# Optimization experiments

Hardware: AMD Instinct MI355X
Metric: run time of the kernel (lower is better)

## Reference

```python
import jax, jax.numpy as jnp
import numpy as np

N_HOST = 50000
N_FLOW = 200000
D = 128
D_OUT = 32
E = 1_000_000
L = 2


def setup_inputs() -> dict:
    key = jax.random.key(0)
    ks = jax.random.split(key, 12)
    s = 0.05  # keep activations well-scaled across layers
    return {
        "x_host": jax.random.normal(ks[0], (N_HOST, D), jnp.float32),
        "x_flow": jax.random.normal(ks[1], (N_FLOW, D), jnp.float32),
        "ehf_src": jax.random.randint(ks[2], (E,), 0, N_HOST),
        "ehf_dst": jax.random.randint(ks[3], (E,), 0, N_FLOW),
        "efh_src": jax.random.randint(ks[4], (E,), 0, N_FLOW),
        "efh_dst": jax.random.randint(ks[5], (E,), 0, N_HOST),
        "Wl": jax.random.normal(ks[6], (L, 2, D, D), jnp.float32) * s,
        "bl": jax.random.normal(ks[7], (L, 2, D), jnp.float32) * s,
        "Wr": jax.random.normal(ks[8], (L, 2, D, D), jnp.float32) * s,
        "br": jax.random.normal(ks[9], (L, 2, D), jnp.float32) * s,
        "W_out": jax.random.normal(ks[10], (D, D_OUT), jnp.float32) * s,
        "b_out": jax.random.normal(ks[11], (D_OUT,), jnp.float32) * s,
    }


def _sage(x_src, x_dst, src, dst, n_dst, wl, bll, wr, brr):
    # SAGEConv (bipartite, mean aggr): lin_l(mean_{j->i} x_src[j]) + lin_r(x_dst[i])
    msg = x_src[src]                                         # [E, D] gather
    agg = jax.ops.segment_sum(msg, dst, num_segments=n_dst)  # [n_dst, D] scatter-add
    cnt = jax.ops.segment_sum(jnp.ones((src.shape[0], 1), x_src.dtype), dst,
                              num_segments=n_dst)
    mean = agg / jnp.maximum(cnt, 1.0)
    return mean @ wl + bll + x_dst @ wr + brr


def reference(x_host, x_flow, ehf_src, ehf_dst, efh_src, efh_dst,
              Wl, bl, Wr, br, W_out, b_out):
    h, f = x_host, x_flow
    for l in range(L):
        # ('host','to','flow') -> updates flow; ('flow','to','host') -> updates host
        nf = _sage(h, f, ehf_src, ehf_dst, N_FLOW, Wl[l, 0], bl[l, 0], Wr[l, 0], br[l, 0])
        nh = _sage(f, h, efh_src, efh_dst, N_HOST, Wl[l, 1], bl[l, 1], Wr[l, 1], br[l, 1])
        f = jax.nn.leaky_relu(nf)  # negative_slope 0.01, matches F.leaky_relu default
        h = jax.nn.leaky_relu(nh)
    return f @ W_out + b_out
```

## Files before the change

kernel.cpp:

```cpp
#include <hip/hip_runtime.h>
#include <stdint.h>

#define N_HOST 50000
#define N_FLOW 200000
#define DIM 128
#define DOUTN 32
#define NEDGE 1000000
#define NLAYER 2

#define GSH_F 8
#define GSH_H 6
#define NB_F ((N_FLOW + (1 << GSH_F) - 1) >> GSH_F)
#define NB_H ((N_HOST + (1 << GSH_H) - 1) >> GSH_H)
#define BCAP 2048
#define AST 136

#define CAST_FBLK 25000
#define CAST_HBLK 6250
#define ZOFF  (CAST_FBLK + CAST_HBLK)
#define ZBLK  13
#define RW_OFF (ZOFF + ZBLK)
#define RO_OFF (RW_OFF + 64)
#define PREP_GRID (RO_OFF + 2)

typedef __bf16 bf16;
typedef __bf16 bf16x4 __attribute__((ext_vector_type(4)));
typedef __bf16 bf16x8 __attribute__((ext_vector_type(8)));
typedef float floatx2 __attribute__((ext_vector_type(2)));
typedef float floatx4 __attribute__((ext_vector_type(4)));
typedef int intx4 __attribute__((ext_vector_type(4)));

__global__ __launch_bounds__(256)
void prep_all_k(const float* __restrict__ xf, const float* __restrict__ xh,
                const float* __restrict__ Wl, const float* __restrict__ Wr,
                const float* __restrict__ Wo,
                bf16* __restrict__ fA, bf16* __restrict__ hAB,
                int* __restrict__ bcnt2,
                bf16* __restrict__ WlF, bf16* __restrict__ WrF,
                bf16* __restrict__ WoF) {
    int bid = blockIdx.x;
    int t = threadIdx.x;
    if (bid < CAST_FBLK) {
        int i = (bid * 256 + t) * 4;
        float4 v = *(const float4*)(xf + i);
        bf16x4 o;
        o[0] = (bf16)v.x; o[1] = (bf16)v.y; o[2] = (bf16)v.z; o[3] = (bf16)v.w;
        *(bf16x4*)(fA + i) = o;
    } else if (bid < ZOFF) {
        int i = ((bid - CAST_FBLK) * 256 + t) * 4;
        float4 v = *(const float4*)(xh + i);
        bf16x4 o;
        o[0] = (bf16)v.x; o[1] = (bf16)v.y; o[2] = (bf16)v.z; o[3] = (bf16)v.w;
        int row = i >> 7, col = i & 127;
        *(bf16x4*)(hAB + row * 256 + col) = o;
    } else if (bid < RW_OFF) {
        int base = (bid - ZOFF) * 2048;
#pragma unroll
        for (int j = 0; j < 8; ++j) {
            int i = base + j * 256 + t;
            if (i < (NB_F + NB_H) * 16) bcnt2[i] = 0;
        }
    } else if (bid < RO_OFF) {
        int b = bid - RW_OFF;
        int y = b >> 3;
        int x = b & 7;
        int lane = t & 63;
        int w = x * 4 + (t >> 6);
        int ct = w >> 2, k0q = w & 3;
        int quad = lane >> 4, m = lane & 15;
        int mat = y & 3;
        const float* W = (y < 4 ? Wl : Wr) + (size_t)mat * DIM * DIM;
        bf16* out = (y < 4 ? WlF : WrF) + (size_t)mat * DIM * DIM;
        bf16x8 o;
#pragma unroll
        for (int j = 0; j < 8; ++j) o[j] = (bf16)W[(k0q * 32 + quad * 8 + j) * DIM + ct * 16 + m];
        *(bf16x8*)(out + ((ct * 4 + k0q) * 64 + lane) * 8) = o;
    } else {
        int b2 = bid - RO_OFF;
        int lane = t & 63;
        int w = b2 * 4 + (t >> 6);
        int ct = w >> 2, k0q = w & 3;
        int quad = lane >> 4, m = lane & 15;
        bf16x8 o;
#pragma unroll
        for (int j = 0; j < 8; ++j) o[j] = (bf16)Wo[(k0q * 32 + quad * 8 + j) * DOUTN + ct * 16 + m];
        *(bf16x8*)(WoF + ((ct * 4 + k0q) * 64 + lane) * 8) = o;
    }
}

__global__ __launch_bounds__(256)
void bucket_scatter2_k(const int* __restrict__ sF, const int* __restrict__ dF,
                       const int* __restrict__ sH, const int* __restrict__ dH,
                       int* bcntF, int* bcntH,
                       int* __restrict__ bkF, int* __restrict__ bkH) {
    int dir = blockIdx.y;
    const int* src = dir ? sH : sF;
    const int* dst = dir ? dH : dF;
    int* bcnt = dir ? bcntH : bcntF;
    int* bkey = dir ? bkH : bkF;
    int gsh = dir ? GSH_H : GSH_F;
    int e = blockIdx.x * 256 + threadIdx.x;
    if (e < NEDGE) {
        int d = dst[e];
        int b = d >> gsh;
        int p = atomicAdd(&bcnt[b << 4], 1);
        if (p < BCAP) bkey[(b << 11) + p] = (src[e] << 8) | (d & ((1 << gsh) - 1));
    }
}

__global__ __launch_bounds__(256)
void bucket_sort2_k(const int* __restrict__ bcntF, const int* __restrict__ bcntH,
                    const int* __restrict__ bkF, const int* __restrict__ bkH,
                    int2* __restrict__ rsF2, int2* __restrict__ rsH2,
                    int* __restrict__ esF, int* __restrict__ esH) {
    __shared__ int cnts[256];
    __shared__ int sd[256];
    __shared__ int ldsout[BCAP];
    int dir = blockIdx.y;
    const int* bcnt = dir ? bcntH : bcntF;
    const int* bkey = dir ? bkH : bkF;
    int2* rs2 = dir ? rsH2 : rsF2;
    int* es = dir ? esH : esF;
    int gsh = dir ? GSH_H : GSH_F;
    int b = blockIdx.x, t = threadIdx.x;
    int G = 1 << gsh;
    int base = b << 11;
    int cnt = bcnt[b << 4];
    if (cnt > BCAP) cnt = BCAP;
    int keys[8]; int nk = 0;
    for (int i = t; i < cnt; i += 256) keys[nk++] = bkey[base + i];
    cnts[t] = 0;
    __syncthreads();
    for (int j = 0; j < nk; ++j) atomicAdd(&cnts[keys[j] & 255], 1);
    __syncthreads();
    int v = cnts[t];
    int x = v;
    sd[t] = x; __syncthreads();
    for (int o = 1; o < 256; o <<= 1) {
        int y = (t >= o) ? sd[t - o] : 0;
        __syncthreads();
        x += y; sd[t] = x; __syncthreads();
    }
    int ex = x - v;
    if (t < G) rs2[(b << gsh) + t] = make_int2(base + ex, base + ex + v);
    cnts[t] = ex;
    __syncthreads();
    for (int j = 0; j < nk; ++j) {
        int k = keys[j];
        int p = atomicAdd(&cnts[k & 255], 1);
        ldsout[p] = k >> 8;
    }
    __syncthreads();
    for (int i = t; i < cnt; i += 256) es[base + i] = ldsout[i];
}

__device__ __forceinline__ void acc_pk4(floatx2* acc, intx4 v) {
    uint32_t d[4] = {(uint32_t)v.x, (uint32_t)v.y, (uint32_t)v.z, (uint32_t)v.w};
#pragma unroll
    for (int k = 0; k < 4; ++k) {
        floatx2 u;
        u.x = __uint_as_float(d[k] << 16);
        u.y = __uint_as_float(d[k] & 0xffff0000u);
        asm("v_pk_add_f32 %0, %1, %0" : "+v"(acc[k]) : "v"(u));
    }
}

#define LRELU(v) ((v) > 0.f ? (v) : 0.01f * (v))

__global__ __launch_bounds__(512, 8)
void host_fused(const int2* __restrict__ rs2, const int* __restrict__ csr,
                const intx4* __restrict__ x4,
                const bf16* __restrict__ hA,
                const bf16* __restrict__ W1f, const bf16* __restrict__ W2f,
                const float* __restrict__ b1, const float* __restrict__ b2,
                bf16* __restrict__ hB) {
    __shared__ __align__(16) bf16 TM[16 * AST];
    int t = threadIdx.x;
    int lane = t & 63, wv = t >> 6;
    int row0 = blockIdx.x << 4;
    {
        int c = lane & 15;
        int q = lane >> 4;
        int half = q & 1;
        int sub = q >> 1;
        int r = row0 + wv * 2 + sub;
        int2 se = rs2[r];
        floatx2 a2[4];
#pragma unroll
        for (int k = 0; k < 4; ++k) a2[k] = (floatx2){0.f, 0.f};
        int e = se.x + half;
        for (; e + 2 < se.y; e += 4) {
            int s0 = csr[e], s1 = csr[e + 2];
            intx4 v0 = x4[s0 * 16 + c];
            intx4 v1 = x4[s1 * 16 + c];
            acc_pk4(a2, v0); acc_pk4(a2, v1);
        }
        if (e < se.y) {
            int s = csr[e];
            intx4 v = x4[s * 16 + c];
            acc_pk4(a2, v);
        }
#pragma unroll
        for (int k = 0; k < 4; ++k) {
            a2[k].x += __shfl_xor(a2[k].x, 16, 64);
            a2[k].y += __shfl_xor(a2[k].y, 16, 64);
        }
        if (half == 0) {
            int deg = se.y - se.x;
            float inv = 1.0f / (float)(deg > 0 ? deg : 1);
            bf16x8 o;
#pragma unroll
            for (int k = 0; k < 4; ++k) {
                o[2 * k]     = (bf16)(a2[k].x * inv);
                o[2 * k + 1] = (bf16)(a2[k].y * inv);
            }
            *(bf16x8*)(TM + (wv * 2 + sub) * AST + c * 8) = o;
        }
    }
    __syncthreads();
    int quad = lane >> 4, m = lane & 15;
    int ccol = wv * 16 + m;
    floatx4 acc = {0.f, 0.f, 0.f, 0.f};
    {
        bf16x8 B[4];
#pragma unroll
        for (int k = 0; k < 4; ++k)
            B[k] = *(const bf16x8*)(W1f + ((wv * 4 + k) * 64 + lane) * 8);
#pragma unroll
        for (int k = 0; k < 4; ++k) {
            bf16x8 a = *(const bf16x8*)(TM + m * AST + quad * 8 + k * 32);
            acc = __builtin_amdgcn_mfma_f32_16x16x32_bf16(a, B[k], acc, 0, 0, 0);
        }
#pragma unroll
        for (int k = 0; k < 4; ++k)
            B[k] = *(const bf16x8*)(W2f + ((wv * 4 + k) * 64 + lane) * 8);
#pragma unroll
        for (int k = 0; k < 4; ++k) {
            bf16x8 a = *(const bf16x8*)(hA + (size_t)(row0 + m) * 256 + quad * 8 + k * 32);
            acc = __builtin_amdgcn_mfma_f32_16x16x32_bf16(a, B[k], acc, 0, 0, 0);
        }
    }
    float bias = b1[ccol] + b2[ccol];
#pragma unroll
    for (int r4 = 0; r4 < 4; ++r4) {
        int row = row0 + quad * 4 + r4;
        float v0 = acc[r4] + bias;
        hB[(size_t)row * 256 + ccol] = (bf16)LRELU(v0);
    }
}

__global__ __launch_bounds__(512, 8)
void flow_fused(const int2* __restrict__ rs2, const int* __restrict__ csr,
                const intx4* __restrict__ tab,
                const bf16* __restrict__ fA,
                const bf16* __restrict__ Wl0f, const bf16* __restrict__ Wr0f,
                const bf16* __restrict__ Wl2f, const bf16* __restrict__ Wr2f,
                const float* __restrict__ bl0, const float* __restrict__ br0,
                const float* __restrict__ bl2, const float* __restrict__ br2,
                const bf16* __restrict__ Wof, const float* __restrict__ bo,
                float* __restrict__ outf) {
    __shared__ __align__(16) bf16 T0[64 * AST];
    __shared__ __align__(16) bf16 T1[64 * AST];
    int t = threadIdx.x;
    int row0 = blockIdx.x << 6;
    {
        int q = t >> 4, c = t & 15;
#pragma unroll
        for (int p = 0; p < 2; ++p) {
            int lr = p * 32 + q;
            int r = row0 + lr;
            int2 se = rs2[r];
            int s0 = se.x, s1 = se.y;
            floatx2 a2[4], b2[4];
#pragma unroll
            for (int k = 0; k < 4; ++k) { a2[k] = (floatx2){0.f, 0.f}; b2[k] = (floatx2){0.f, 0.f}; }
            for (int e = s0; e < s1; ++e) {
                int sa = csr[e];
                intx4 va = tab[sa * 32 + c];
                intx4 vb = tab[sa * 32 + 16 + c];
                acc_pk4(a2, va); acc_pk4(b2, vb);
            }
            int deg = s1 - s0;
            float inv = 1.0f / (float)(deg > 0 ? deg : 1);
            bf16x8 oa, ob;
#pragma unroll
            for (int k = 0; k < 4; ++k) {
                oa[2 * k]     = (bf16)(a2[k].x * inv);
                oa[2 * k + 1] = (bf16)(a2[k].y * inv);
                ob[2 * k]     = (bf16)(b2[k].x * inv);
                ob[2 * k + 1] = (bf16)(b2[k].y * inv);
            }
            *(bf16x8*)(T0 + lr * AST + c * 8) = oa;
            *(bf16x8*)(T1 + lr * AST + c * 8) = ob;
        }
    }
    __syncthreads();
    int lane = t & 63, wv = t >> 6;
    int quad = lane >> 4, m = lane & 15;
    int ccol = wv * 16 + m;
    floatx4 zero4 = {0.f, 0.f, 0.f, 0.f};
    floatx4 acc[4];
#pragma unroll
    for (int rt = 0; rt < 4; ++rt) acc[rt] = zero4;
    {
        bf16x8 B[4];
#pragma unroll
        for (int k = 0; k < 4; ++k)
            B[k] = *(const bf16x8*)(Wl0f + ((wv * 4 + k) * 64 + lane) * 8);
#pragma unroll
        for (int rt = 0; rt < 4; ++rt)
#pragma unroll
            for (int k = 0; k < 4; ++k) {
                bf16x8 a = *(const bf16x8*)(T0 + (rt * 16 + m) * AST + quad * 8 + k * 32);
                acc[rt] = __builtin_amdgcn_mfma_f32_16x16x32_bf16(a, B[k], acc[rt], 0, 0, 0);
            }
#pragma unroll
        for (int k = 0; k < 4; ++k)
            B[k] = *(const bf16x8*)(Wr0f + ((wv * 4 + k) * 64 + lane) * 8);
#pragma unroll
        for (int rt = 0; rt < 4; ++rt)
#pragma unroll
            for (int k = 0; k < 4; ++k) {
                bf16x8 a = *(const bf16x8*)(fA + (size_t)(row0 + rt * 16 + m) * DIM + quad * 8 + k * 32);
                acc[rt] = __builtin_amdgcn_mfma_f32_16x16x32_bf16(a, B[k], acc[rt], 0, 0, 0);
            }
    }
    {
        float bias = bl0[ccol] + br0[ccol];
        __syncthreads();
#pragma unroll
        for (int rt = 0; rt < 4; ++rt)
#pragma unroll
            for (int r4 = 0; r4 < 4; ++r4) {
                int lr = rt * 16 + quad * 4 + r4;
                float v0 = acc[rt][r4] + bias;
                T0[lr * AST + ccol] = (bf16)LRELU(v0);
            }
        __syncthreads();
    }
#pragma unroll
    for (int rt = 0; rt < 4; ++rt) acc[rt] = zero4;
    {
        bf16x8 B[4];
#pragma unroll
        for (int k = 0; k < 4; ++k)
            B[k] = *(const bf16x8*)(Wl2f + ((wv * 4 + k) * 64 + lane) * 8);
#pragma unroll
        for (int rt = 0; rt < 4; ++rt)
#pragma unroll
            for (int k = 0; k < 4; ++k) {
                bf16x8 a = *(const bf16x8*)(T1 + (rt * 16 + m) * AST + quad * 8 + k * 32);
                acc[rt] = __builtin_amdgcn_mfma_f32_16x16x32_bf16(a, B[k], acc[rt], 0, 0, 0);
            }
#pragma unroll
        for (int k = 0; k < 4; ++k)
            B[k] = *(const bf16x8*)(Wr2f + ((wv * 4 + k) * 64 + lane) * 8);
#pragma unroll
        for (int rt = 0; rt < 4; ++rt)
#pragma unroll
            for (int k = 0; k < 4; ++k) {
                bf16x8 a = *(const bf16x8*)(T0 + (rt * 16 + m) * AST + quad * 8 + k * 32);
                acc[rt] = __builtin_amdgcn_mfma_f32_16x16x32_bf16(a, B[k], acc[rt], 0, 0, 0);
            }
    }
    {
        float bias = bl2[ccol] + br2[ccol];
        __syncthreads();
#pragma unroll
        for (int rt = 0; rt < 4; ++rt)
#pragma unroll
            for (int r4 = 0; r4 < 4; ++r4) {
                int lr = rt * 16 + quad * 4 + r4;
                float v0 = acc[rt][r4] + bias;
                T1[lr * AST + ccol] = (bf16)LRELU(v0);
            }
        __syncthreads();
    }
    {
        int s = wv >> 1, h = wv & 1;
        bf16x8 BO[4];
#pragma unroll
        for (int k = 0; k < 4; ++k)
            BO[k] = *(const bf16x8*)(Wof + ((h * 4 + k) * 64 + lane) * 8);
        floatx4 o = zero4;
        const bf16* fp = T1 + (s * 16 + m) * AST + quad * 8;
#pragma unroll
        for (int k = 0; k < 4; ++k) {
            bf16x8 af = *(const bf16x8*)(fp + k * 32);
            o = __builtin_amdgcn_mfma_f32_16x16x32_bf16(af, BO[k], o, 0, 0, 0);
        }
        float bov = bo[h * 16 + m];
#pragma unroll
        for (int r = 0; r < 4; ++r) {
            int row = row0 + s * 16 + quad * 4 + r;
            outf[row * DOUTN + h * 16 + m] = o[r] + bov;
        }
    }
}

extern "C" void kernel_launch(void* const* d_in, const int* in_sizes, int n_in,
                              void* d_out, int out_size, void* d_ws, size_t ws_size,
                              hipStream_t stream) {
    (void)in_sizes; (void)n_in; (void)out_size; (void)ws_size;
    const float* x_host  = (const float*)d_in[0];
    const float* x_flow  = (const float*)d_in[1];
    const int*   ehf_src = (const int*)d_in[2];
    const int*   ehf_dst = (const int*)d_in[3];
    const int*   efh_src = (const int*)d_in[4];
    const int*   efh_dst = (const int*)d_in[5];
    const float* Wl      = (const float*)d_in[6];
    const float* bl      = (const float*)d_in[7];
    const float* Wr      = (const float*)d_in[8];
    const float* br      = (const float*)d_in[9];
    const float* W_out   = (const float*)d_in[10];
    const float* b_out   = (const float*)d_in[11];
    float* out = (float*)d_out;

    char* basep = (char*)d_ws;
    size_t off = 0;
    auto alloc = [&](size_t b) -> void* {
        void* p = basep + off;
        off += (b + 255) & ~(size_t)255;
        return p;
    };

    bf16* fA     = (bf16*)alloc((size_t)N_FLOW * DIM * 2);
    bf16* hAB    = (bf16*)alloc((size_t)N_HOST * 256 * 2);
    bf16* WlF    = (bf16*)alloc((size_t)NLAYER * 2 * DIM * DIM * 2);
    bf16* WrF    = (bf16*)alloc((size_t)NLAYER * 2 * DIM * DIM * 2);
    bf16* WoF    = (bf16*)alloc((size_t)DIM * DOUTN * 2);

    int* bcnt2   = (int*)alloc((size_t)(NB_F + NB_H) * 16 * 4);
    int* bcntF   = bcnt2;
    int* bcntH   = bcnt2 + NB_F * 16;
    int* bkF     = (int*)alloc((size_t)NB_F * BCAP * 4);
    int* bkH     = (int*)alloc((size_t)NB_H * BCAP * 4);
    int* esF     = (int*)alloc((size_t)NB_F * BCAP * 4);
    int* esH     = (int*)alloc((size_t)NB_H * BCAP * 4);
    int2* rsF2   = (int2*)alloc((size_t)NB_F * (1 << GSH_F) * 8);
    int2* rsH2   = (int2*)alloc((size_t)NB_H * (1 << GSH_H) * 8);

    prep_all_k<<<PREP_GRID, 256, 0, stream>>>(
        x_flow, x_host, Wl, Wr, W_out, fA, hAB, bcnt2, WlF, WrF, WoF);

    bucket_scatter2_k<<<dim3((NEDGE + 255) / 256, 2), 256, 0, stream>>>(
        ehf_src, ehf_dst, efh_src, efh_dst, bcntF, bcntH, bkF, bkH);

    bucket_sort2_k<<<dim3(NB_F, 2), 256, 0, stream>>>(
        bcntF, bcntH, bkF, bkH, rsF2, rsH2, esF, esH);

    host_fused<<<N_HOST / 16, 512, 0, stream>>>(
        rsH2, esH, (const intx4*)fA, hAB,
        WlF + 1 * DIM * DIM, WrF + 1 * DIM * DIM,
        bl + 1 * DIM, br + 1 * DIM, hAB + 128);

    flow_fused<<<N_FLOW / 64, 512, 0, stream>>>(
        rsF2, esF, (const intx4*)hAB, fA,
        WlF + 0 * DIM * DIM, WrF + 0 * DIM * DIM,
        WlF + 2 * DIM * DIM, WrF + 2 * DIM * DIM,
        bl + 0 * DIM, br + 0 * DIM, bl + 2 * DIM, br + 2 * DIM,
        WoF, b_out, out);
}
```

Measured before the change: 499.5 us.

## Fuse per-bucket CSR sort into host/flow consumer kernels via LDS counting sort

Removes the separate bucket_sort kernel and its esF/esH/rs arrays. Buckets are resized to match consumer block rows (16 host rows, 64 flow rows, capacity 1024), and each consumer block counting-sorts its own bucket keys in LDS before gathering. This saves a kernel launch and a global write/read pass over the sorted edges, at the cost of extra LDS use and syncs in the fused kernels. A bucket holding more than 1024 edges would silently drop edges; the expected count is 320 per bucket, so overflow is unlikely.

After: 487.2 us. 1.03x faster.

```diff
diff --git a/kernel.cpp b/kernel.cpp
--- a/kernel.cpp
+++ b/kernel.cpp
@@ -8,17 +8,16 @@
 #define NEDGE 1000000
 #define NLAYER 2
 
-#define GSH_F 8
-#define GSH_H 6
-#define NB_F ((N_FLOW + (1 << GSH_F) - 1) >> GSH_F)
-#define NB_H ((N_HOST + (1 << GSH_H) - 1) >> GSH_H)
-#define BCAP 2048
+#define GSH_F 6
+#define GSH_H 4
+#define NBUCK 3125
+#define BCAP 1024
 #define AST 136
 
 #define CAST_FBLK 25000
 #define CAST_HBLK 6250
 #define ZOFF  (CAST_FBLK + CAST_HBLK)
-#define ZBLK  13
+#define ZBLK  49
 #define RW_OFF (ZOFF + ZBLK)
 #define RO_OFF (RW_OFF + 64)
 #define PREP_GRID (RO_OFF + 2)
@@ -58,7 +57,7 @@
 #pragma unroll
         for (int j = 0; j < 8; ++j) {
             int i = base + j * 256 + t;
-            if (i < (NB_F + NB_H) * 16) bcnt2[i] = 0;
+            if (i < 2 * NBUCK * 16) bcnt2[i] = 0;
         }
     } else if (bid < RO_OFF) {
         int b = bid - RW_OFF;
@@ -104,54 +103,8 @@
         int d = dst[e];
         int b = d >> gsh;
         int p = atomicAdd(&bcnt[b << 4], 1);
-        if (p < BCAP) bkey[(b << 11) + p] = (src[e] << 8) | (d & ((1 << gsh) - 1));
-    }
-}
-
-__global__ __launch_bounds__(256)
-void bucket_sort2_k(const int* __restrict__ bcntF, const int* __restrict__ bcntH,
-                    const int* __restrict__ bkF, const int* __restrict__ bkH,
-                    int2* __restrict__ rsF2, int2* __restrict__ rsH2,
-                    int* __restrict__ esF, int* __restrict__ esH) {
-    __shared__ int cnts[256];
-    __shared__ int sd[256];
-    __shared__ int ldsout[BCAP];
-    int dir = blockIdx.y;
-    const int* bcnt = dir ? bcntH : bcntF;
-    const int* bkey = dir ? bkH : bkF;
-    int2* rs2 = dir ? rsH2 : rsF2;
-    int* es = dir ? esH : esF;
-    int gsh = dir ? GSH_H : GSH_F;
-    int b = blockIdx.x, t = threadIdx.x;
-    int G = 1 << gsh;
-    int base = b << 11;
-    int cnt = bcnt[b << 4];
-    if (cnt > BCAP) cnt = BCAP;
-    int keys[8]; int nk = 0;
-    for (int i = t; i < cnt; i += 256) keys[nk++] = bkey[base + i];
-    cnts[t] = 0;
-    __syncthreads();
-    for (int j = 0; j < nk; ++j) atomicAdd(&cnts[keys[j] & 255], 1);
-    __syncthreads();
-    int v = cnts[t];
-    int x = v;
-    sd[t] = x; __syncthreads();
-    for (int o = 1; o < 256; o <<= 1) {
-        int y = (t >= o) ? sd[t - o] : 0;
-        __syncthreads();
-        x += y; sd[t] = x; __syncthreads();
-    }
-    int ex = x - v;
-    if (t < G) rs2[(b << gsh) + t] = make_int2(base + ex, base + ex + v);
-    cnts[t] = ex;
-    __syncthreads();
-    for (int j = 0; j < nk; ++j) {
-        int k = keys[j];
-        int p = atomicAdd(&cnts[k & 255], 1);
-        ldsout[p] = k >> 8;
-    }
-    __syncthreads();
-    for (int i = t; i < cnt; i += 256) es[base + i] = ldsout[i];
+        if (p < BCAP) bkey[(b << 10) + p] = (src[e] << 8) | (d & ((1 << gsh) - 1));
+    }
 }
 
 __device__ __forceinline__ void acc_pk4(floatx2* acc, intx4 v) {
@@ -168,35 +121,64 @@
 #define LRELU(v) ((v) > 0.f ? (v) : 0.01f * (v))
 
 __global__ __launch_bounds__(512, 8)
-void host_fused(const int2* __restrict__ rs2, const int* __restrict__ csr,
+void host_fused(const int* __restrict__ bcnt, const int* __restrict__ bkey,
                 const intx4* __restrict__ x4,
                 const bf16* __restrict__ hA,
                 const bf16* __restrict__ W1f, const bf16* __restrict__ W2f,
                 const float* __restrict__ b1, const float* __restrict__ b2,
                 bf16* __restrict__ hB) {
     __shared__ __align__(16) bf16 TM[16 * AST];
+    __shared__ int ek[BCAP];
+    __shared__ int rstart[17];
+    __shared__ int rcur[16];
     int t = threadIdx.x;
     int lane = t & 63, wv = t >> 6;
-    int row0 = blockIdx.x << 4;
+    int b = blockIdx.x;
+    int row0 = b << 4;
+    int cnt = bcnt[b << 4];
+    if (cnt > BCAP) cnt = BCAP;
+    int k0 = (t < cnt) ? bkey[(b << 10) + t] : -1;
+    int k1 = (t + 512 < cnt) ? bkey[(b << 10) + t + 512] : -1;
+    if (t < 16) rcur[t] = 0;
+    __syncthreads();
+    if (k0 >= 0) atomicAdd(&rcur[k0 & 15], 1);
+    if (k1 >= 0) atomicAdd(&rcur[k1 & 15], 1);
+    __syncthreads();
+    if (t < 16) {
+        int v = rcur[t];
+        int x = v;
+#pragma unroll
+        for (int o = 1; o < 16; o <<= 1) {
+            int y = __shfl_up(x, o, 64);
+            if (t >= o) x += y;
+        }
+        rstart[t] = x - v;
+        rcur[t] = x - v;
+        if (t == 15) rstart[16] = x;
+    }
+    __syncthreads();
+    if (k0 >= 0) { int p = atomicAdd(&rcur[k0 & 15], 1); ek[p] = k0 >> 8; }
+    if (k1 >= 0) { int p = atomicAdd(&rcur[k1 & 15], 1); ek[p] = k1 >> 8; }
+    __syncthreads();
     {
         int c = lane & 15;
         int q = lane >> 4;
         int half = q & 1;
         int sub = q >> 1;
-        int r = row0 + wv * 2 + sub;
-        int2 se = rs2[r];
+        int lr = wv * 2 + sub;
+        int s0 = rstart[lr], s1 = rstart[lr + 1];
         floatx2 a2[4];
 #pragma unroll
         for (int k = 0; k < 4; ++k) a2[k] = (floatx2){0.f, 0.f};
-        int e = se.x + half;
-        for (; e + 2 < se.y; e += 4) {
-            int s0 = csr[e], s1 = csr[e + 2];
-            intx4 v0 = x4[s0 * 16 + c];
-            intx4 v1 = x4[s1 * 16 + c];
+        int e = s0 + half;
+        for (; e + 2 < s1; e += 4) {
+            int i0 = ek[e], i1 = ek[e + 2];
+            intx4 v0 = x4[i0 * 16 + c];
+            intx4 v1 = x4[i1 * 16 + c];
             acc_pk4(a2, v0); acc_pk4(a2, v1);
         }
-        if (e < se.y) {
-            int s = csr[e];
+        if (e < s1) {
+            int s = ek[e];
             intx4 v = x4[s * 16 + c];
             acc_pk4(a2, v);
         }
@@ -206,7 +188,7 @@
             a2[k].y += __shfl_xor(a2[k].y, 16, 64);
         }
         if (half == 0) {
-            int deg = se.y - se.x;
+            int deg = s1 - s0;
             float inv = 1.0f / (float)(deg > 0 ? deg : 1);
             bf16x8 o;
 #pragma unroll
@@ -214,7 +196,7 @@
                 o[2 * k]     = (bf16)(a2[k].x * inv);
                 o[2 * k + 1] = (bf16)(a2[k].y * inv);
             }
-            *(bf16x8*)(TM + (wv * 2 + sub) * AST + c * 8) = o;
+            *(bf16x8*)(TM + lr * AST + c * 8) = o;
         }
     }
     __syncthreads();
@@ -250,7 +232,7 @@
 }
 
 __global__ __launch_bounds__(512, 8)
-void flow_fused(const int2* __restrict__ rs2, const int* __restrict__ csr,
+void flow_fused(const int* __restrict__ bcnt, const int* __restrict__ bkey,
                 const intx4* __restrict__ tab,
                 const bf16* __restrict__ fA,
                 const bf16* __restrict__ Wl0f, const bf16* __restrict__ Wr0f,
@@ -261,21 +243,48 @@
                 float* __restrict__ outf) {
     __shared__ __align__(16) bf16 T0[64 * AST];
     __shared__ __align__(16) bf16 T1[64 * AST];
+    __shared__ int ek[BCAP];
+    __shared__ int rstart[65];
+    __shared__ int rcur[64];
     int t = threadIdx.x;
-    int row0 = blockIdx.x << 6;
+    int b = blockIdx.x;
+    int row0 = b << 6;
+    int cnt = bcnt[b << 4];
+    if (cnt > BCAP) cnt = BCAP;
+    int k0 = (t < cnt) ? bkey[(b << 10) + t] : -1;
+    int k1 = (t + 512 < cnt) ? bkey[(b << 10) + t + 512] : -1;
+    if (t < 64) rcur[t] = 0;
+    __syncthreads();
+    if (k0 >= 0) atomicAdd(&rcur[k0 & 63], 1);
+    if (k1 >= 0) atomicAdd(&rcur[k1 & 63], 1);
+    __syncthreads();
+    if (t < 64) {
+        int v = rcur[t];
+        int x = v;
+#pragma unroll
+        for (int o = 1; o < 64; o <<= 1) {
+            int y = __shfl_up(x, o, 64);
+            if (t >= o) x += y;
+        }
+        rstart[t] = x - v;
+        rcur[t] = x - v;
+        if (t == 63) rstart[64] = x;
+    }
+    __syncthreads();
+    if (k0 >= 0) { int p = atomicAdd(&rcur[k0 & 63], 1); ek[p] = k0 >> 8; }
+    if (k1 >= 0) { int p = atomicAdd(&rcur[k1 & 63], 1); ek[p] = k1 >> 8; }
+    __syncthreads();
     {
         int q = t >> 4, c = t & 15;
 #pragma unroll
         for (int p = 0; p < 2; ++p) {
             int lr = p * 32 + q;
-            int r = row0 + lr;
-            int2 se = rs2[r];
-            int s0 = se.x, s1 = se.y;
+            int s0 = rstart[lr], s1 = rstart[lr + 1];
             floatx2 a2[4], b2[4];
 #pragma unroll
             for (int k = 0; k < 4; ++k) { a2[k] = (floatx2){0.f, 0.f}; b2[k] = (floatx2){0.f, 0.f}; }
             for (int e = s0; e < s1; ++e) {
-                int sa = csr[e];
+                int sa = ek[e];
                 intx4 va = tab[sa * 32 + c];
                 intx4 vb = tab[sa * 32 + 16 + c];
                 acc_pk4(a2, va); acc_pk4(b2, vb);
@@ -430,15 +439,11 @@
     bf16* WrF    = (bf16*)alloc((size_t)NLAYER * 2 * DIM * DIM * 2);
     bf16* WoF    = (bf16*)alloc((size_t)DIM * DOUTN * 2);
 
-    int* bcnt2   = (int*)alloc((size_t)(NB_F + NB_H) * 16 * 4);
+    int* bcnt2   = (int*)alloc((size_t)2 * NBUCK * 16 * 4);
     int* bcntF   = bcnt2;
-    int* bcntH   = bcnt2 + NB_F * 16;
-    int* bkF     = (int*)alloc((size_t)NB_F * BCAP * 4);
-    int* bkH     = (int*)alloc((size_t)NB_H * BCAP * 4);
-    int* esF     = (int*)alloc((size_t)NB_F * BCAP * 4);
-    int* esH     = (int*)alloc((size_t)NB_H * BCAP * 4);
-    int2* rsF2   = (int2*)alloc((size_t)NB_F * (1 << GSH_F) * 8);
-    int2* rsH2   = (int2*)alloc((size_t)NB_H * (1 << GSH_H) * 8);
+    int* bcntH   = bcnt2 + NBUCK * 16;
+    int* bkF     = (int*)alloc((size_t)NBUCK * BCAP * 4);
+    int* bkH     = (int*)alloc((size_t)NBUCK * BCAP * 4);
 
     prep_all_k<<<PREP_GRID, 256, 0, stream>>>(
         x_flow, x_host, Wl, Wr, W_out, fA, hAB, bcnt2, WlF, WrF, WoF);
@@ -446,16 +451,13 @@
     bucket_scatter2_k<<<dim3((NEDGE + 255) / 256, 2), 256, 0, stream>>>(
         ehf_src, ehf_dst, efh_src, efh_dst, bcntF, bcntH, bkF, bkH);
 
-    bucket_sort2_k<<<dim3(NB_F, 2), 256, 0, stream>>>(
-        bcntF, bcntH, bkF, bkH, rsF2, rsH2, esF, esH);
-
-    host_fused<<<N_HOST / 16, 512, 0, stream>>>(
-        rsH2, esH, (const intx4*)fA, hAB,
+    host_fused<<<NBUCK, 512, 0, stream>>>(
+        bcntH, bkH, (const intx4*)fA, hAB,
         WlF + 1 * DIM * DIM, WrF + 1 * DIM * DIM,
         bl + 1 * DIM, br + 1 * DIM, hAB + 128);
 
-    flow_fused<<<N_FLOW / 64, 512, 0, stream>>>(
-        rsF2, esF, (const intx4*)hAB, fA,
+    flow_fused<<<NBUCK, 512, 0, stream>>>(
+        bcntF, bkF, (const intx4*)hAB, fA,
         WlF + 0 * DIM * DIM, WrF + 0 * DIM * DIM,
         WlF + 2 * DIM * DIM, WrF + 2 * DIM * DIM,
         bl + 0 * DIM, br + 0 * DIM, bl + 2 * DIM, br + 2 * DIM,
```
